# Kernel optimization log

Hardware: AMD Instinct MI355X
Metric: run time of the kernel (lower is better)

Reference implementation:

```python
import jax, jax.numpy as jnp
import numpy as np

SL, BS, OUT_SL = 64, 64, 48
NH, EME, EMD = 256, 512, 768   # em_sz_dec == 3*NH required by copy-score reshape/bmm
VE, VD = 32000, 32000
NL = 2


def setup_inputs() -> dict:
    key = jax.random.key(0)
    ks = iter(jax.random.split(key, 32))
    def W(*s, sc=0.05):
        return jax.random.normal(next(ks), s, jnp.float32) * sc
    inp = jax.random.randint(next(ks), (SL, BS), 0, VE)
    y = jax.random.randint(next(ks), (SL, BS), 0, VD)
    return dict(
        inp=inp, y=y,
        emb_enc=W(VE, EME, sc=0.1),
        enc_Wih=W(NL, 2, 3 * NH, EME), enc_Whh=W(NL, 2, 3 * NH, NH),
        enc_bih=W(NL, 2, 3 * NH), enc_bhh=W(NL, 2, 3 * NH),
        out_enc_W=W(EMD, 2 * NH),
        emb_dec=W(VD, EMD, sc=0.1),
        dec_Wih=W(NL, 3 * EMD, EMD), dec_Whh=W(NL, 3 * EMD, EMD),
        dec_bih=W(NL, 3 * EMD), dec_bhh=W(NL, 3 * EMD),
        out_b=W(VD),
        W1=W(2 * NH, EMD), l2_W=W(EMD, EMD), l2_b=W(EMD),
        l3_W=W(EMD, EMD + 2 * NH), l3_b=W(EMD),
        Vp=W(EMD),
    )


def _gru_cell(x, h, Wih, Whh, bih, bhh):
    # torch nn.GRU cell equations
    gi = x @ Wih.T + bih
    gh = h @ Whh.T + bhh
    ir, iz, inn = jnp.split(gi, 3, axis=-1)
    hr, hz, hn = jnp.split(gh, 3, axis=-1)
    r = jax.nn.sigmoid(ir + hr)
    z = jax.nn.sigmoid(iz + hz)
    n = jnp.tanh(inn + r * hn)
    return (1.0 - z) * n + z * h


def _gru_layer(xs, h0, Wih, Whh, bih, bhh, reverse=False):
    def step(h, x):
        h2 = _gru_cell(x, h, Wih, Whh, bih, bhh)
        return h2, h2
    hT, ys = jax.lax.scan(step, h0, xs, reverse=reverse)
    return ys, hT


def reference(inp, y, emb_enc, enc_Wih, enc_Whh, enc_bih, enc_bhh, out_enc_W,
              emb_dec, dec_Wih, dec_Whh, dec_bih, dec_bhh, out_b,
              W1, l2_W, l2_b, l3_W, l3_b, Vp):
    sl, bs = inp.shape
    # ---- encoder: 2-layer bidirectional GRU ----
    x = emb_enc[inp]                                   # (sl, bs, EME)
    h_fin = []
    for l in range(NL):
        yf, hf = _gru_layer(x, jnp.zeros((bs, NH), x.dtype),
                            enc_Wih[l, 0], enc_Whh[l, 0], enc_bih[l, 0], enc_bhh[l, 0])
        yb, hb = _gru_layer(x, jnp.zeros((bs, NH), x.dtype),
                            enc_Wih[l, 1], enc_Whh[l, 1], enc_bih[l, 1], enc_bhh[l, 1],
                            reverse=True)
        x = jnp.concatenate([yf, yb], -1)              # (sl, bs, 2*NH)
        h_fin.append(jnp.concatenate([hf, hb], -1))    # (bs, 2*NH)
    enc_out = x
    # h.view(2,2,bs,-1).permute(0,2,1,3).view(2,bs,-1) == per-layer [fwd,bwd] concat
    h = jnp.stack(h_fin) @ out_enc_W.T                 # (2, bs, EMD)

    w1e = enc_out @ W1                                 # (sl, bs, EMD)
    sc_base = jnp.tanh(enc_out @ out_enc_W.T).transpose(1, 0, 2)  # (bs, sl, EMD)
    yT = y.T                                           # (bs, sl) copy indices
    Vsz = emb_dec.shape[0]
    row = jnp.arange(bs)[:, None]
    # dec_inp: step 0 uses zeros token, then teacher-forced y[i-1]
    dec_inputs = jnp.concatenate([jnp.zeros((1, bs), y.dtype), y[:OUT_SL - 1]], 0)

    def step(h, dec_t):
        # Bahdanau attention
        w2h = h[-1] @ l2_W.T + l2_b                    # (bs, EMD)
        u = jnp.tanh(w1e + w2h[None])                  # (sl, bs, EMD)
        a = jax.nn.softmax(u @ Vp, axis=0)             # (sl, bs)
        Xa = jnp.einsum('sb,sbe->be', a, enc_out)      # (bs, 2*NH)
        e = emb_dec[dec_t]                             # (bs, EMD)
        wgt = jnp.concatenate([e, Xa], -1) @ l3_W.T + l3_b
        # 2-layer decoder GRU, single step
        h0n = _gru_cell(wgt, h[0], dec_Wih[0], dec_Whh[0], dec_bih[0], dec_bhh[0])
        h1n = _gru_cell(h0n, h[1], dec_Wih[1], dec_Whh[1], dec_bih[1], dec_bhh[1])
        hn = jnp.stack([h0n, h1n])
        dec_out = h1n                                  # (bs, EMD)
        outp = dec_out @ emb_dec.T + out_b             # generate scores (bs, VD), tied weights
        score_c = jnp.tanh(jnp.einsum('bse,be->bs', sc_base, dec_out))  # copy scores (bs, sl)
        probs = jax.nn.softmax(jnp.concatenate([outp, score_c], 1), axis=1)  # (bs, VD+sl)
        prob_g = probs[:, :Vsz]
        prob_c = probs[:, Vsz:]
        # scatter-add copy probs onto the token ids of y (the copy mechanism)
        out1 = jnp.zeros_like(probs).at[row, yT].add(prob_c)
        out1 = out1.at[:, :Vsz].add(prob_g)
        return hn, out1

    _, res = jax.lax.scan(step, h, dec_inputs)         # (OUT_SL, bs, VD+sl)
    return res
```

## Files before the change

kernel.cpp:

```cpp
#include <hip/hip_runtime.h>

#define SLEN 64
#define BSZ  64
#define TSL  48
#define VDIM 32000
#define NCOL 32064

typedef __attribute__((ext_vector_type(8))) _Float16 f16x8;
typedef __attribute__((ext_vector_type(4))) _Float16 f16x4;
typedef __attribute__((ext_vector_type(4))) float f32x4;

__device__ __forceinline__ float fsig(float x){
    return 1.0f/(1.0f + __expf(-x));
}
__device__ __forceinline__ float ftanh(float x){
    float e = __expf(2.0f*x);
    return 1.0f - 2.0f/(e + 1.0f);
}
__device__ __forceinline__ unsigned short f2h(float x){
    union { _Float16 f; unsigned short u; } c; c.f = (_Float16)x; return c.u;
}
__device__ __forceinline__ float h2f(unsigned short u){
    union { _Float16 f; unsigned short u; } c; c.u = u; return (float)c.f;
}
__device__ __forceinline__ unsigned short f2h_hi(float x, float& rem){
    _Float16 h = (_Float16)x;
    rem = x - (float)h;
    union { _Float16 f; unsigned short u; } c; c.f = h; return c.u;
}
__device__ __forceinline__ float gru_fuse(float gir,float giz,float gin,
                                          float ghr,float ghz,float ghn,float h){
    float r = fsig(gir + ghr);
    float z = fsig(giz + ghz);
    float n = ftanh(gin + r*ghn);
    return (1.0f - z)*n + z*h;
}

__global__ __launch_bounds__(256) void mfma_gemm(
    const float* A0, const unsigned short* Bh0, const unsigned short* Bl0,
    const float* bias0, float* C0, int N0, int ldc0, int act0,
    const float* A1, const unsigned short* Bh1, const unsigned short* Bl1,
    const float* bias1, float* C1, int N1, int ldc1, int act1,
    int K, int c16)
{
    const float* A; const unsigned short* Bh; const unsigned short* Bl;
    const float* bias; float* C; int N, ldc, act;
    if (blockIdx.z == 0) { A=A0; Bh=Bh0; Bl=Bl0; bias=bias0; C=C0; N=N0; ldc=ldc0; act=act0; }
    else                 { A=A1; Bh=Bh1; Bl=Bl1; bias=bias1; C=C1; N=N1; ldc=ldc1; act=act1; }

    const int n0 = blockIdx.x * 128;
    if (n0 >= N) return;
    const int m0 = blockIdx.y * 64;

    __shared__ __align__(16) unsigned short As[2][64][72];
    __shared__ __align__(16) unsigned short Bs[2][128][72];

    const int t  = threadIdx.x;
    const int wv = t >> 6, ln = t & 63;
    const bool has_lo = (Bl != nullptr);

    f32x4 acc[4][2];
    #pragma unroll
    for (int i = 0; i < 4; ++i)
        #pragma unroll
        for (int j = 0; j < 2; ++j) acc[i][j] = (f32x4){0.f,0.f,0.f,0.f};

    for (int k0 = 0; k0 < K; k0 += 64) {
        __syncthreads();
        #pragma unroll
        for (int it = 0; it < 4; ++it) {
            int idx = t + it*256;
            int r = idx >> 4, c4 = (idx & 15) * 4;
            float4 v = *reinterpret_cast<const float4*>(A + (size_t)(m0+r)*K + k0 + c4);
            ushort4 h, l; float rm;
            h.x = f2h_hi(v.x, rm); l.x = f2h(rm);
            h.y = f2h_hi(v.y, rm); l.y = f2h(rm);
            h.z = f2h_hi(v.z, rm); l.z = f2h(rm);
            h.w = f2h_hi(v.w, rm); l.w = f2h(rm);
            *reinterpret_cast<ushort4*>(&As[0][r][c4]) = h;
            *reinterpret_cast<ushort4*>(&As[1][r][c4]) = l;
        }
        #pragma unroll
        for (int it = 0; it < 4; ++it) {
            int idx = t + it*256;
            int r = idx >> 3, c8 = (idx & 7) * 8;
            *reinterpret_cast<uint4*>(&Bs[0][r][c8]) =
                *reinterpret_cast<const uint4*>(&Bh[(size_t)(n0+r)*K + k0 + c8]);
        }
        if (has_lo) {
            #pragma unroll
            for (int it = 0; it < 4; ++it) {
                int idx = t + it*256;
                int r = idx >> 3, c8 = (idx & 7) * 8;
                *reinterpret_cast<uint4*>(&Bs[1][r][c8]) =
                    *reinterpret_cast<const uint4*>(&Bl[(size_t)(n0+r)*K + k0 + c8]);
            }
        }
        __syncthreads();
        #pragma unroll
        for (int ks = 0; ks < 2; ++ks) {
            const int ko = ks*32 + (ln >> 4)*8;
            f16x8 ah[4], al[4], bh[2], bl[2];
            #pragma unroll
            for (int m = 0; m < 4; ++m) {
                ah[m] = *reinterpret_cast<const f16x8*>(&As[0][m*16 + (ln&15)][ko]);
                al[m] = *reinterpret_cast<const f16x8*>(&As[1][m*16 + (ln&15)][ko]);
            }
            #pragma unroll
            for (int n = 0; n < 2; ++n) {
                bh[n] = *reinterpret_cast<const f16x8*>(&Bs[0][wv*32 + n*16 + (ln&15)][ko]);
                if (has_lo)
                    bl[n] = *reinterpret_cast<const f16x8*>(&Bs[1][wv*32 + n*16 + (ln&15)][ko]);
            }
            #pragma unroll
            for (int m = 0; m < 4; ++m)
                #pragma unroll
                for (int n = 0; n < 2; ++n) {
                    acc[m][n] = __builtin_amdgcn_mfma_f32_16x16x32_f16(ah[m], bh[n], acc[m][n], 0,0,0);
                    acc[m][n] = __builtin_amdgcn_mfma_f32_16x16x32_f16(al[m], bh[n], acc[m][n], 0,0,0);
                    if (has_lo)
                        acc[m][n] = __builtin_amdgcn_mfma_f32_16x16x32_f16(ah[m], bl[n], acc[m][n], 0,0,0);
                }
        }
    }
    #pragma unroll
    for (int m = 0; m < 4; ++m) {
        #pragma unroll
        for (int n = 0; n < 2; ++n) {
            const int col = n0 + wv*32 + n*16 + (ln & 15);
            const float bz = bias ? bias[col] : 0.0f;
            #pragma unroll
            for (int j = 0; j < 4; ++j) {
                const int row = m0 + m*16 + (ln >> 4)*4 + j;
                float v = acc[m][n][j] + bz;
                if (act) v = ftanh(v);
                if (c16) ((unsigned short*)C)[(size_t)row*ldc + col] = f2h(v);
                else     C[(size_t)row*ldc + col] = v;
            }
        }
    }
}

__global__ __launch_bounds__(256) void packwhh_k(
    const float* __restrict__ Whh, unsigned short* __restrict__ P)
{
    int gidx = blockIdx.x*256 + threadIdx.x;
    if (gidx >= 2*3*32*256) return;
    int col = gidx & 255;
    int k8  = (gidx >> 8) & 31;
    int g   = (gidx >> 13) % 3;
    int d   = gidx / (3*32*256);
    const float* src = Whh + ((size_t)(d*768 + g*256 + col))*256 + k8*8;
    ushort4 lo4, hi4;
    float4 v0 = *reinterpret_cast<const float4*>(src);
    float4 v1 = *reinterpret_cast<const float4*>(src + 4);
    lo4.x = f2h(v0.x); lo4.y = f2h(v0.y); lo4.z = f2h(v0.z); lo4.w = f2h(v0.w);
    hi4.x = f2h(v1.x); hi4.y = f2h(v1.y); hi4.z = f2h(v1.z); hi4.w = f2h(v1.w);
    reinterpret_cast<ushort4*>(P + (size_t)gidx*8)[0] = lo4;
    reinterpret_cast<ushort4*>(P + (size_t)gidx*8)[1] = hi4;
}

__global__ __launch_bounds__(512) void enc_cp5_k(
    const float* __restrict__ giF, const float* __restrict__ giB,
    const unsigned short* __restrict__ Wp,
    const float* __restrict__ bhh,
    float* __restrict__ yout, float* __restrict__ hfin, int permute)
{
    const int b = blockIdx.x, d = blockIdx.y, t = threadIdx.x;
    const int c  = t & 255;
    const int kh = t >> 8;
    const float* gi_base = d ? giB : giF;
    const unsigned short* W = Wp + (size_t)d*3*32*256*8;
    const float br  = bhh[d*768 + c];
    const float bz2 = bhh[d*768 + c + 256];
    const float bn  = bhh[d*768 + c + 512];

    __shared__ float hsA[256];
    __shared__ float hsB[256];
    __shared__ float red[3][256];
    if (kh == 0) hsA[c] = 0.0f;

    float gr = 0.f, gz = 0.f, gn = 0.f, h_own = 0.f;
    if (kh == 0) {
        const int s0 = d ? 63 : 0;
        const float* gip0 = gi_base + (size_t)(s0*64 + b)*768;
        gr = gip0[c]; gz = gip0[c+256]; gn = gip0[c+512];
    }
    __syncthreads();

    for (int step = 0; step < 64; ++step) {
        const int s = d ? (63 - step) : step;
        float ngr = 0.f, ngz = 0.f, ngn = 0.f;
        if (kh == 0 && step < 63) {
            const int sn = d ? (62 - step) : (step + 1);
            const float* gip = gi_base + (size_t)(sn*64 + b)*768;
            ngr = gip[c]; ngz = gip[c+256]; ngn = gip[c+512];
        }
        const float* hs = (step & 1) ? hsB : hsA;
        float*       hw = (step & 1) ? hsA : hsB;

        float ar = 0.f, az = 0.f, an = 0.f;
        const int kb = kh * 16;
        #pragma unroll 8
        for (int k8i = 0; k8i < 16; ++k8i) {
            const int k8 = kb + k8i;
            f16x8 wr = *reinterpret_cast<const f16x8*>(W + ((size_t)(0*32 + k8)*256 + c)*8);
            f16x8 wz = *reinterpret_cast<const f16x8*>(W + ((size_t)(1*32 + k8)*256 + c)*8);
            f16x8 wn = *reinterpret_cast<const f16x8*>(W + ((size_t)(2*32 + k8)*256 + c)*8);
            float4 h0 = *reinterpret_cast<const float4*>(&hs[k8*8]);
            float4 h1 = *reinterpret_cast<const float4*>(&hs[k8*8+4]);
            ar += h0.x*(float)wr[0] + h0.y*(float)wr[1] + h0.z*(float)wr[2] + h0.w*(float)wr[3]
                + h1.x*(float)wr[4] + h1.y*(float)wr[5] + h1.z*(float)wr[6] + h1.w*(float)wr[7];
            az += h0.x*(float)wz[0] + h0.y*(float)wz[1] + h0.z*(float)wz[2] + h0.w*(float)wz[3]
                + h1.x*(float)wz[4] + h1.y*(float)wz[5] + h1.z*(float)wz[6] + h1.w*(float)wz[7];
            an += h0.x*(float)wn[0] + h0.y*(float)wn[1] + h0.z*(float)wn[2] + h0.w*(float)wn[3]
                + h1.x*(float)wn[4] + h1.y*(float)wn[5] + h1.z*(float)wn[6] + h1.w*(float)wn[7];
        }
        if (kh == 1) { red[0][c] = ar; red[1][c] = az; red[2][c] = an; }
        __syncthreads();
        if (kh == 0) {
            ar += red[0][c]; az += red[1][c]; an += red[2][c];
            float r  = fsig(gr + ar + br);
            float z  = fsig(gz + az + bz2);
            float n  = ftanh(gn + r*(an + bn));
            float hn2 = (1.0f - z)*n + z*h_own;
            h_own = hn2;
            hw[c] = hn2;
            const int idx = permute ? (b*64 + s) : (s*64 + b);
            yout[(size_t)idx*512 + d*256 + c] = hn2;
            gr = ngr; gz = ngz; gn = ngn;
        }
        __syncthreads();
    }
    if (kh == 0) hfin[(size_t)b*512 + d*256 + c] = h_own;
}

__global__ __launch_bounds__(512) void gru_mfma_k(
    const float* A0, const unsigned short* BH0, const unsigned short* BL0,
    const float* bias0, const float* gh0, const float* hold0, float* out0,
    int gate0, int K0, const unsigned short* E0,
    const float* A1, const unsigned short* BH1, const unsigned short* BL1,
    const float* bias1, const float* gh1, const float* hold1, float* out1,
    int gate1, int K1, const unsigned short* E1, float* psz)
{
    const float* A; const unsigned short* BH; const unsigned short* BL;
    const float* bias; const float* gh; const float* hold; float* outp; int gate, K;
    const unsigned short* E;
    if (blockIdx.z == 0) { A=A0; BH=BH0; BL=BL0; bias=bias0; gh=gh0; hold=hold0; outp=out0; gate=gate0; K=K0; E=E0; }
    else                 { A=A1; BH=BH1; BL=BL1; bias=bias1; gh=gh1; hold=hold1; outp=out1; gate=gate1; K=K1; E=E1; }

    const int t = threadIdx.x;
    if (psz && blockIdx.z == 0 && blockIdx.x == 0) psz[t] = 0.f;
    const int w  = t >> 6, ln = t & 63;
    const int rw = w & 3;
    const int kh = w >> 2;
    const int colg16 = blockIdx.x * 16;
    const int arow = rw*16 + (ln & 15);
    const int kof  = (ln >> 4) * 8;
    const bool has_lo = (BL != nullptr);

    f32x4 acc[3];
    #pragma unroll
    for (int g = 0; g < 3; ++g) acc[g] = (f32x4){0.f,0.f,0.f,0.f};

    const float* Ar = A + (size_t)arow*K + kof;
    const int brow_n = colg16 + (ln & 15);
    const int Khalf = K >> 1;
    const int kbeg = kh * Khalf;

    #pragma unroll 2
    for (int k0 = kbeg; k0 < kbeg + Khalf; k0 += 32) {
        float4 a0 = *reinterpret_cast<const float4*>(Ar + k0);
        float4 a1 = *reinterpret_cast<const float4*>(Ar + k0 + 4);
        f16x8 ah, al;
        {
            float av0=a0.x, av1=a0.y, av2=a0.z, av3=a0.w;
            float av4=a1.x, av5=a1.y, av6=a1.z, av7=a1.w;
            _Float16 hh;
            hh=(_Float16)av0; ah[0]=hh; al[0]=(_Float16)(av0-(float)hh);
            hh=(_Float16)av1; ah[1]=hh; al[1]=(_Float16)(av1-(float)hh);
            hh=(_Float16)av2; ah[2]=hh; al[2]=(_Float16)(av2-(float)hh);
            hh=(_Float16)av3; ah[3]=hh; al[3]=(_Float16)(av3-(float)hh);
            hh=(_Float16)av4; ah[4]=hh; al[4]=(_Float16)(av4-(float)hh);
            hh=(_Float16)av5; ah[5]=hh; al[5]=(_Float16)(av5-(float)hh);
            hh=(_Float16)av6; ah[6]=hh; al[6]=(_Float16)(av6-(float)hh);
            hh=(_Float16)av7; ah[7]=hh; al[7]=(_Float16)(av7-(float)hh);
        }
        #pragma unroll
        for (int g = 0; g < 3; ++g) {
            const size_t boff = (size_t)(g*768 + brow_n)*K + k0 + kof;
            f16x8 bh = *reinterpret_cast<const f16x8*>(&BH[boff]);
            acc[g] = __builtin_amdgcn_mfma_f32_16x16x32_f16(ah, bh, acc[g], 0,0,0);
            acc[g] = __builtin_amdgcn_mfma_f32_16x16x32_f16(al, bh, acc[g], 0,0,0);
            if (has_lo) {
                f16x8 bl = *reinterpret_cast<const f16x8*>(&BL[boff]);
                acc[g] = __builtin_amdgcn_mfma_f32_16x16x32_f16(ah, bl, acc[g], 0,0,0);
            }
        }
    }

    __shared__ float red[4][64][12];
    if (kh == 1) {
        #pragma unroll
        for (int g = 0; g < 3; ++g)
            #pragma unroll
            for (int j = 0; j < 4; ++j) red[rw][ln][g*4 + j] = acc[g][j];
    }
    __syncthreads();
    if (kh == 1) return;
    #pragma unroll
    for (int g = 0; g < 3; ++g)
        #pragma unroll
        for (int j = 0; j < 4; ++j) acc[g][j] += red[rw][ln][g*4 + j];

    const int colg = colg16 + (ln & 15);
    const int rb   = rw*16 + (ln >> 4)*4;
    if (gate) {
        const float br = bias[colg], bz = bias[768+colg], bn = bias[1536+colg];
        #pragma unroll
        for (int jj = 0; jj < 4; ++jj) {
            const int row = rb + jj;
            float er = 0.f, ez = 0.f, en = 0.f;
            if (E) {
                er = h2f(E[(size_t)row*2304 + colg]);
                ez = h2f(E[(size_t)row*2304 + 768 + colg]);
                en = h2f(E[(size_t)row*2304 + 1536 + colg]);
            }
            float ghr = gh[(size_t)row*2304 + colg];
            float ghz = gh[(size_t)row*2304 + 768 + colg];
            float ghn = gh[(size_t)row*2304 + 1536 + colg];
            float h   = hold[(size_t)row*768 + colg];
            outp[(size_t)row*768 + colg] =
                gru_fuse(acc[0][jj]+br+er, acc[1][jj]+bz+ez, acc[2][jj]+bn+en, ghr, ghz, ghn, h);
        }
    } else {
        #pragma unroll
        for (int g = 0; g < 3; ++g) {
            const float bz = bias[g*768 + colg];
            #pragma unroll
            for (int jj = 0; jj < 4; ++jj)
                outp[(size_t)(rb+jj)*2304 + g*768 + colg] = acc[g][jj] + bz;
        }
    }
}

__global__ __launch_bounds__(512) void vocab4_k(
    const float* __restrict__ A,
    const unsigned short* __restrict__ B0, const float* __restrict__ bias0,
    unsigned short* __restrict__ scr16, float* __restrict__ psum,
    const unsigned short* __restrict__ B1, const float* __restrict__ bias1, float* __restrict__ C1,
    const unsigned short* __restrict__ B2, const float* __restrict__ bias2, float* __restrict__ C2,
    const unsigned short* __restrict__ scb16, float* __restrict__ cpt)
{
    const int z = blockIdx.z;
    const int t = threadIdx.x, w = t >> 6, ln = t & 63;

    if (z == 3) {
        const int b = blockIdx.x;
        if (b >= 64) return;
        __shared__ float hsh[768];
        for (int i = t; i < 768; i += 512) hsh[i] = A[(size_t)b*768 + i];
        __syncthreads();
        for (int ss = 0; ss < 8; ++ss) {
            const int s = w*8 + ss;
            const unsigned short* sp = scb16 + (size_t)(b*64 + s)*768;
            float acc = 0.f;
            #pragma unroll
            for (int q = 0; q < 6; ++q) {
                int e = ln*2 + q*128;
                unsigned u = *reinterpret_cast<const unsigned*>(&sp[e]);
                acc += h2f((unsigned short)(u & 0xffff))*hsh[e]
                     + h2f((unsigned short)(u >> 16))*hsh[e+1];
            }
            for (int off = 32; off; off >>= 1) acc += __shfl_down(acc, off);
            if (ln == 0) cpt[b*64 + s] = ftanh(acc);
        }
        return;
    }

    const unsigned short* Bh; const float* bias; int N, ldc;
    if (z == 0)      { Bh=B0; bias=bias0; N=VDIM; ldc=VDIM; }
    else if (z == 1) { Bh=B1; bias=bias1; N=768;  ldc=768; }
    else             { Bh=B2; bias=bias2; N=2304; ldc=2304; }
    const int n0 = blockIdx.x * 128;
    if (n0 >= N) return;

    __shared__ __align__(16) unsigned short As[2][64][72];
    __shared__ __align__(16) unsigned short Bs[128][72];
    __shared__ float rs[4][64];

    const int cw = w & 3;
    const int mh = w >> 2;

    f32x4 acc[2][2];
    #pragma unroll
    for (int i = 0; i < 2; ++i)
        #pragma unroll
        for (int j = 0; j < 2; ++j) acc[i][j] = (f32x4){0.f,0.f,0.f,0.f};

    for (int k0 = 0; k0 < 768; k0 += 64) {
        __syncthreads();
        #pragma unroll
        for (int it = 0; it < 2; ++it) {
            int idx = t + it*512;
            int r = idx >> 4, c4 = (idx & 15) * 4;
            float4 v = *reinterpret_cast<const float4*>(A + (size_t)r*768 + k0 + c4);
            ushort4 h, l; float rm;
            h.x = f2h_hi(v.x, rm); l.x = f2h(rm);
            h.y = f2h_hi(v.y, rm); l.y = f2h(rm);
            h.z = f2h_hi(v.z, rm); l.z = f2h(rm);
            h.w = f2h_hi(v.w, rm); l.w = f2h(rm);
            *reinterpret_cast<ushort4*>(&As[0][r][c4]) = h;
            *reinterpret_cast<ushort4*>(&As[1][r][c4]) = l;
        }
        #pragma unroll
        for (int it = 0; it < 2; ++it) {
            int idx = t + it*512;
            int r = idx >> 3, c8 = (idx & 7) * 8;
            *reinterpret_cast<uint4*>(&Bs[r][c8]) =
                *reinterpret_cast<const uint4*>(&Bh[(size_t)(n0+r)*768 + k0 + c8]);
        }
        __syncthreads();
        #pragma unroll
        for (int ks = 0; ks < 2; ++ks) {
            const int ko = ks*32 + (ln >> 4)*8;
            f16x8 ah[2], al[2], bh[2];
            #pragma unroll
            for (int m = 0; m < 2; ++m) {
                ah[m] = *reinterpret_cast<const f16x8*>(&As[0][mh*32 + m*16 + (ln&15)][ko]);
                al[m] = *reinterpret_cast<const f16x8*>(&As[1][mh*32 + m*16 + (ln&15)][ko]);
            }
            #pragma unroll
            for (int n = 0; n < 2; ++n)
                bh[n] = *reinterpret_cast<const f16x8*>(&Bs[cw*32 + n*16 + (ln&15)][ko]);
            #pragma unroll
            for (int m = 0; m < 2; ++m)
                #pragma unroll
                for (int n = 0; n < 2; ++n) {
                    acc[m][n] = __builtin_amdgcn_mfma_f32_16x16x32_f16(ah[m], bh[n], acc[m][n], 0,0,0);
                    acc[m][n] = __builtin_amdgcn_mfma_f32_16x16x32_f16(al[m], bh[n], acc[m][n], 0,0,0);
                }
        }
    }

    if (z == 0) {
        __syncthreads();
        unsigned short (*Cs)[128] = reinterpret_cast<unsigned short(*)[128]>(&As[0][0][0]);
        float sums[2][4];
        #pragma unroll
        for (int m = 0; m < 2; ++m)
            #pragma unroll
            for (int j = 0; j < 4; ++j) sums[m][j] = 0.f;
        #pragma unroll
        for (int m = 0; m < 2; ++m) {
            #pragma unroll
            for (int n = 0; n < 2; ++n) {
                const int cl = cw*32 + n*16 + (ln & 15);
                const float bz = bias[n0 + cl];
                #pragma unroll
                for (int j = 0; j < 4; ++j) {
                    const int row = mh*32 + m*16 + (ln >> 4)*4 + j;
                    float e = __expf(acc[m][n][j] + bz);
                    Cs[row][cl] = f2h(e);
                    sums[m][j] += e;
                }
            }
        }
        #pragma unroll
        for (int m = 0; m < 2; ++m)
            #pragma unroll
            for (int j = 0; j < 4; ++j) {
                float v = sums[m][j];
                v += __shfl_xor(v, 1); v += __shfl_xor(v, 2);
                v += __shfl_xor(v, 4); v += __shfl_xor(v, 8);
                if ((ln & 15) == 0)
                    rs[cw][mh*32 + m*16 + (ln >> 4)*4 + j] = v;
            }
        __syncthreads();
        #pragma unroll
        for (int it = 0; it < 2; ++it) {
            int jj = t + it*512;
            int row = jj >> 4, c8 = (jj & 15) * 8;
            *reinterpret_cast<uint4*>(&scr16[(size_t)row*VDIM + n0 + c8]) =
                *reinterpret_cast<const uint4*>(&Cs[row][c8]);
        }
        if (t < 64)
            atomicAdd(&psum[t*8 + (blockIdx.x & 7)], rs[0][t]+rs[1][t]+rs[2][t]+rs[3][t]);
    } else {
        float* C = (z == 1) ? C1 : C2;
        #pragma unroll
        for (int m = 0; m < 2; ++m) {
            #pragma unroll
            for (int n = 0; n < 2; ++n) {
                const int col = n0 + cw*32 + n*16 + (ln & 15);
                const float bz = bias[col];
                #pragma unroll
                for (int j = 0; j < 4; ++j) {
                    const int row = mh*32 + m*16 + (ln >> 4)*4 + j;
                    C[(size_t)row*ldc + col] = acc[m][n][j] + bz;
                }
            }
        }
    }
}

__global__ __launch_bounds__(512) void attsm_k(
    const unsigned short* __restrict__ w1e16, const float* __restrict__ w2h,
    const float* __restrict__ Vp, const unsigned short* __restrict__ enc16,
    const int* __restrict__ y,
    int step, int do_att, int do_sm,
    float* __restrict__ wgt_in,
    const unsigned short* __restrict__ scr16, const float* __restrict__ cpt,
    const float* __restrict__ psum, float* __restrict__ outprev)
{
    const int b = blockIdx.x, t = threadIdx.x;
    const int w = t >> 6, ln = t & 63;
    if (blockIdx.y == 0) {
        if (!do_att) return;
        __shared__ float w2s[768];
        __shared__ float vps[768];
        __shared__ float aa[64];
        for (int i = t; i < 768; i += 512) { w2s[i] = w2h[(size_t)b*768 + i]; vps[i] = Vp[i]; }
        __syncthreads();
        for (int ss = 0; ss < 8; ++ss) {
            const int s = w*8 + ss;
            const unsigned short* wrow = w1e16 + (size_t)(b*64 + s)*768;
            float acc = 0.f;
            #pragma unroll
            for (int q = 0; q < 6; ++q) {
                int e = ln*2 + q*128;
                unsigned u = *reinterpret_cast<const unsigned*>(&wrow[e]);
                acc += ftanh(h2f((unsigned short)(u & 0xffff)) + w2s[e])*vps[e]
                     + ftanh(h2f((unsigned short)(u >> 16))   + w2s[e+1])*vps[e+1];
            }
            for (int off = 32; off; off >>= 1) acc += __shfl_down(acc, off);
            if (ln == 0) aa[s] = acc;
        }
        __syncthreads();
        if (t < 64) {
            float v = aa[t];
            float m = v;
            for (int off = 32; off; off >>= 1) m = fmaxf(m, __shfl_xor(m, off));
            float e = __expf(v - m);
            float ssum = e;
            for (int off = 32; off; off >>= 1) ssum += __shfl_xor(ssum, off);
            aa[t] = e / ssum;
        }
        __syncthreads();
        {
            float a0 = 0.f;
            const unsigned short* ebase = enc16 + (size_t)(b*64)*512 + t;
            #pragma unroll 8
            for (int s = 0; s < 64; ++s)
                a0 += aa[s] * h2f(ebase[(size_t)s*512]);
            wgt_in[(size_t)b*512 + t] = a0;
        }
    } else {
        if (!do_sm) return;
        __shared__ float cps[64];
        __shared__ float invS;
        if (t < 64) cps[t] = __expf(cpt[b*64 + t]);
        __syncthreads();
        if (t < 64) {
            float v = cps[t];
            for (int off = 32; off; off >>= 1) v += __shfl_xor(v, off);
            if (t == 0) {
                float tot = v;
                #pragma unroll
                for (int k = 0; k < 8; ++k) tot += psum[b*8 + k];
                invS = 1.0f / tot;
            }
        }
        __syncthreads();
        const float inv = invS;
        const unsigned short* srow = scr16 + (size_t)b*VDIM;
        float* orow = outprev + (size_t)b*NCOL;
        for (int i = t*8; i < VDIM; i += 4096) {
            uint4 u = *reinterpret_cast<const uint4*>(&srow[i]);
            float4 o0, o1;
            o0.x = h2f((unsigned short)(u.x & 0xffff))*inv; o0.y = h2f((unsigned short)(u.x >> 16))*inv;
            o0.z = h2f((unsigned short)(u.y & 0xffff))*inv; o0.w = h2f((unsigned short)(u.y >> 16))*inv;
            o1.x = h2f((unsigned short)(u.z & 0xffff))*inv; o1.y = h2f((unsigned short)(u.z >> 16))*inv;
            o1.z = h2f((unsigned short)(u.w & 0xffff))*inv; o1.w = h2f((unsigned short)(u.w >> 16))*inv;
            *reinterpret_cast<float4*>(&orow[i])     = o0;
            *reinterpret_cast<float4*>(&orow[i + 4]) = o1;
        }
        if (t >= 448) orow[VDIM + (t - 448)] = 0.0f;
        __syncthreads();
        if (t < 64) atomicAdd(&orow[y[t*64 + b]], cps[t] * inv);
    }
}

__global__ __launch_bounds__(256) void convhl_k(
    const float* __restrict__ W, unsigned short* __restrict__ hi,
    unsigned short* __restrict__ lo, int n4)
{
    int i = blockIdx.x*256 + threadIdx.x;
    if (i >= n4) return;
    float4 v = reinterpret_cast<const float4*>(W)[i];
    ushort4 h, l; float r;
    h.x = f2h_hi(v.x, r); l.x = f2h(r);
    h.y = f2h_hi(v.y, r); l.y = f2h(r);
    h.z = f2h_hi(v.z, r); l.z = f2h(r);
    h.w = f2h_hi(v.w, r); l.w = f2h(r);
    reinterpret_cast<ushort4*>(hi)[i] = h;
    reinterpret_cast<ushort4*>(lo)[i] = l;
}
__global__ __launch_bounds__(256) void conv16_k(
    const float* __restrict__ W, unsigned short* __restrict__ hi, int n4)
{
    int i = blockIdx.x*256 + threadIdx.x;
    if (i >= n4) return;
    float4 v = reinterpret_cast<const float4*>(W)[i];
    ushort4 h;
    h.x = f2h(v.x); h.y = f2h(v.y); h.z = f2h(v.z); h.w = f2h(v.w);
    reinterpret_cast<ushort4*>(hi)[i] = h;
}
__global__ __launch_bounds__(256) void convw03_k(
    const float* __restrict__ W03f, unsigned short* __restrict__ We,
    unsigned short* __restrict__ Wx)
{
    int i = blockIdx.x*256 + threadIdx.x;
    if (i >= 2304*320) return;
    int r = i / 320, c4 = (i - r*320) * 4;
    float4 v = *reinterpret_cast<const float4*>(W03f + (size_t)r*1280 + c4);
    ushort4 h;
    h.x = f2h(v.x); h.y = f2h(v.y); h.z = f2h(v.z); h.w = f2h(v.w);
    if (c4 < 768)
        *reinterpret_cast<ushort4*>(&We[(size_t)r*768 + c4]) = h;
    else
        *reinterpret_cast<ushort4*>(&Wx[(size_t)r*512 + (c4 - 768)]) = h;
}
__global__ __launch_bounds__(256) void embrows_k(
    const int* __restrict__ y, const float* __restrict__ emb_dec,
    float* __restrict__ Ag)
{
    int i = blockIdx.x*256 + threadIdx.x;
    if (i >= 3072*192) return;
    int row = i / 192, c4 = (i - row*192) * 4;
    int tok = (row < 64) ? 0 : y[row - 64];
    *reinterpret_cast<float4*>(Ag + (size_t)row*768 + c4) =
        *reinterpret_cast<const float4*>(emb_dec + (size_t)tok*768 + c4);
// ... 265 lines not shown
__global__ __launch_bounds__(256) void smax2_k(
    const float* __restrict__ scratch, const float* __restrict__ scb,
    const float* __restrict__ h1, const int* __restrict__ y, float* __restrict__ out)
{
    const int b = blockIdx.x, t = threadIdx.x;
    __shared__ float hsh[768];
    __shared__ float cps[64];
    __shared__ float red[4];
    for (int i = t; i < 768; i += 256) hsh[i] = h1[(size_t)b*768 + i];
    __syncthreads();
    const int wv = t >> 6, ln = t & 63;
    for (int ss = 0; ss < 16; ++ss) {
        const int s = wv*16 + ss;
        const float* sp = scb + (size_t)(b*64 + s)*768;
        float acc = 0.f;
        #pragma unroll
        for (int q = 0; q < 12; ++q) { int e = ln + q*64; acc += sp[e]*hsh[e]; }
        for (int off = 32; off; off >>= 1) acc += __shfl_down(acc, off);
        if (ln == 0) cps[s] = ftanh(acc);
    }
    __syncthreads();

    const float* row = scratch + (size_t)b*VDIM;
    float m = -1e30f;
    for (int i = t; i < VDIM; i += 256) m = fmaxf(m, row[i]);
    for (int off = 32; off; off >>= 1) m = fmaxf(m, __shfl_xor(m, off));
    if (ln == 0) red[wv] = m;
    __syncthreads();
    const float bm = fmaxf(fmaxf(red[0], red[1]), fmaxf(red[2], red[3]));
    __syncthreads();

    float s = 0.f;
    for (int i = t; i < VDIM; i += 256) s += __expf(row[i] - bm);
    if (t < 64) s += __expf(cps[t] - bm);
    for (int off = 32; off; off >>= 1) s += __shfl_xor(s, off);
    if (ln == 0) red[wv] = s;
    __syncthreads();
    const float inv = 1.0f / (red[0] + red[1] + red[2] + red[3]);

    float* orow = out + (size_t)b*NCOL;
    for (int i = t; i < VDIM; i += 256) orow[i] = __expf(row[i] - bm) * inv;
    if (t >= 192) orow[VDIM + (t - 192)] = 0.0f;
    __syncthreads();
    if (t < 64) atomicAdd(&orow[y[t*64 + b]], __expf(cps[t] - bm) * inv);
}

extern "C" void kernel_launch(void* const* d_in, const int* in_sizes, int n_in,
                              void* d_out, int out_size, void* d_ws, size_t ws_size,
                              hipStream_t stream)
{
    (void)in_sizes; (void)n_in; (void)out_size;
    const int*   inp       = (const int*)  d_in[0];
    const int*   y         = (const int*)  d_in[1];
    const float* emb_enc   = (const float*)d_in[2];
    const float* enc_Wih   = (const float*)d_in[3];
    const float* enc_Whh   = (const float*)d_in[4];
    const float* enc_bih   = (const float*)d_in[5];
    const float* enc_bhh   = (const float*)d_in[6];
    const float* out_enc_W = (const float*)d_in[7];
    const float* emb_dec   = (const float*)d_in[8];
    const float* dec_Wih   = (const float*)d_in[9];
    const float* dec_Whh   = (const float*)d_in[10];
    const float* dec_bih   = (const float*)d_in[11];
    const float* dec_bhh   = (const float*)d_in[12];
    const float* out_b     = (const float*)d_in[13];
    const float* W1        = (const float*)d_in[14];
    const float* l2_W      = (const float*)d_in[15];
    const float* l2_b      = (const float*)d_in[16];
    const float* l3_W      = (const float*)d_in[17];
    const float* l3_b      = (const float*)d_in[18];
    const float* Vp        = (const float*)d_in[19];
    float* out = (float*)d_out;
    float* ws  = (float*)d_ws;

    size_t off = 0;
    auto alloc = [&](size_t n) { float* p = ws + off; off += (n + 63) & ~(size_t)63; return p; };
    float* x0     = alloc(4096*512);
    float* x1     = alloc(4096*512);
    float* x2     = alloc(4096*512);
    float* giF    = alloc(4096*768);
    float* giB    = alloc(4096*768);
    float* w1e    = alloc(4096*768);
    float* scb    = alloc(4096*768);
    float* W1T    = alloc(768*512);
    float* hfin   = alloc(128*512);
    float* hdecA  = alloc(128*768);
    float* hdecB  = alloc(128*768);
    float* w2h    = alloc(64*768);
    float* wgt_in = alloc(64*1280);
    float* wgt    = alloc(64*768);
    float* gh0buf = alloc(64*2304);
    float* gh1buf = alloc(64*2304);
    float* gi0f   = alloc(64*2304);
    float* gi1f   = alloc(64*2304);
    float* b03    = alloc(2304);
    float* psum   = alloc(1024);
    float* cpt    = alloc(2*4096);
    float* scratch= alloc(64*VDIM);
    auto ualloc = [&](size_t nush) { return (unsigned short*)alloc((nush + 1) / 2); };
    unsigned short* encWhhH = ualloc(2*2*768*256);
    unsigned short* encWhhP = ualloc(2*3*32*256*8);
    unsigned short* embH    = ualloc((size_t)VDIM*768);
    unsigned short* encWihH = ualloc(2*2*768*512);
    unsigned short* encWihL = ualloc(2*2*768*512);
    unsigned short* W1TH    = ualloc(768*512);
    unsigned short* W1TL    = ualloc(768*512);
    unsigned short* oeH     = ualloc(768*512);
    unsigned short* oeL     = ualloc(768*512);
    unsigned short* l2H     = ualloc(768*768);
    unsigned short* l3TH    = ualloc(1280*768);
    unsigned short* l3TL    = ualloc(1280*768);
    unsigned short* dWihH   = ualloc((size_t)2*2304*768);
    unsigned short* dWhhH   = ualloc((size_t)2*2304*768);
    unsigned short* W03eH   = ualloc((size_t)2304*768);
    unsigned short* W03xH   = ualloc((size_t)2304*512);
    unsigned short* Egi16   = ualloc((size_t)3072*2304);
    const bool use_mfma = ws_size >= off * sizeof(float);

    const size_t L1W = (size_t)2304*768;
    const size_t SCR = (size_t)64*VDIM;
    float* l3T  = scratch;
    float* W03f = x0;
    float* Ag   = x0;
    unsigned short* scr16 = (unsigned short*)scratch;
    unsigned short* w1e16 = (unsigned short*)giF;
    unsigned short* enc16 = (unsigned short*)(giF + 1600*1024);
    unsigned short* scb16 = (unsigned short*)giB;

    embed_k<<<2048, 256, 0, stream>>>(inp, emb_enc, x0);
    transpose2_k<<<(512*768 + 255)/256, 256, 0, stream>>>(W1, W1T, 512, 768);
    conv16_k<<<768, 256, 0, stream>>>(enc_Whh, encWhhH, 2*2*768*256/4);

    if (use_mfma) {
        packwhh_k<<<192, 256, 0, stream>>>(enc_Whh, encWhhP);
        convhl_k<<<1536, 256, 0, stream>>>(enc_Wih, encWihH, encWihL, 2*2*768*512/4);
        convhl_k<<<384, 256, 0, stream>>>(W1T, W1TH, W1TL, 768*512/4);
        convhl_k<<<384, 256, 0, stream>>>(out_enc_W, oeH, oeL, 768*512/4);
        conv16_k<<<576, 256, 0, stream>>>(l2_W, l2H, 768*768/4);
        conv16_k<<<3456, 256, 0, stream>>>(dec_Wih, dWihH, (int)(L1W*2/4));
        conv16_k<<<3456, 256, 0, stream>>>(dec_Whh, dWhhH, (int)(L1W*2/4));
        conv16_k<<<24000, 256, 0, stream>>>(emb_dec, embH, (int)((size_t)VDIM*768/4));
        transpose2_k<<<(768*1280 + 255)/256, 256, 0, stream>>>(l3_W, l3T, 768, 1280);
        convhl_k<<<960, 256, 0, stream>>>(l3T, l3TH, l3TL, 1280*768/4);
        b03_k<<<9, 256, 0, stream>>>(dec_Wih, dec_bih, l3_b, b03);

        for (int l = 0; l < 2; ++l) {
            const float* xin  = l ? x1 : x0;
            float*       xout = l ? x2 : x1;
            const size_t wo = (size_t)l*2*768*512;
            mfma_gemm<<<dim3(6, 64, 2), 256, 0, stream>>>(
                xin, encWihH + wo,           encWihL + wo,           enc_bih + l*2*768,       giF, 768, 768, 0,
                xin, encWihH + wo + 768*512, encWihL + wo + 768*512, enc_bih + l*2*768 + 768, giB, 768, 768, 0,
                512, 0);
            enc_cp5_k<<<dim3(64, 2), 512, 0, stream>>>(
                giF, giB, encWhhP, enc_bhh + (size_t)l*2*768,
                xout, hfin + (size_t)l*64*512, l);
            if (l == 0)
                packwhh_k<<<192, 256, 0, stream>>>(enc_Whh + (size_t)2*768*256, encWhhP);
        }

        mfma_gemm<<<dim3(10, 36, 1), 256, 0, stream>>>(
            dec_Wih, l3TH, l3TL, nullptr, W03f, 1280, 1280, 0,
            nullptr, nullptr, nullptr, nullptr, nullptr, 0, 0, 0,
            768, 0);
        convw03_k<<<(2304*320 + 255)/256, 256, 0, stream>>>(W03f, W03eH, W03xH);

        embrows_k<<<(3072*192 + 255)/256, 256, 0, stream>>>(y, emb_dec, Ag);
        mfma_gemm<<<dim3(18, 48, 1), 256, 0, stream>>>(
            Ag, W03eH, nullptr, nullptr, (float*)Egi16, 2304, 2304, 0,
            nullptr, nullptr, nullptr, nullptr, nullptr, 0, 0, 0,
            768, 1);

        mfma_gemm<<<dim3(6, 2, 1), 256, 0, stream>>>(
            hfin, oeH, oeL, nullptr, hdecA, 768, 768, 0,
            nullptr, nullptr, nullptr, nullptr, nullptr, 0, 0, 0,
            512, 0);

        mfma_gemm<<<dim3(6, 64, 2), 256, 0, stream>>>(
            x2, W1TH, W1TL, nullptr, w1e, 768, 768, 0,
            x2, oeH,  oeL,  nullptr, scb, 768, 768, 1,
            512, 0);

        conv16_k<<<3072, 256, 0, stream>>>(w1e, w1e16, 4096*768/4);
        conv16_k<<<3072, 256, 0, stream>>>(scb, scb16, 4096*768/4);
        conv16_k<<<2048, 256, 0, stream>>>(x2, enc16, 4096*512/4);

        mfma_gemm<<<dim3(6, 1, 1), 256, 0, stream>>>(
            hdecA + 64*768, l2H, nullptr, l2_b, w2h, 768, 768, 0,
            nullptr, nullptr, nullptr, nullptr, nullptr, 0, 0, 0,
            768, 0);
        gru_mfma_k<<<dim3(48, 1, 2), 512, 0, stream>>>(
            hdecA,          dWhhH,       nullptr, dec_bhh,        nullptr, nullptr, gh0buf, 0, 768, nullptr,
            hdecA + 64*768, dWhhH + L1W, nullptr, dec_bhh + 2304, nullptr, nullptr, gh1buf, 0, 768, nullptr,
            nullptr);

        for (int st = 0; st < TSL; ++st) {
            float* h0c = (st & 1) ? hdecB : hdecA;
            float* h0n = (st & 1) ? hdecA : hdecB;
            float* h1c = h0c + 64*768;
            float* h1n = h0n + 64*768;
            float* oprev = out + (size_t)(st > 0 ? st - 1 : 0)*BSZ*NCOL;

            attsm_k<<<dim3(64, 2), 512, 0, stream>>>(
                w1e16, w2h, Vp, enc16, y, st, 1, (st > 0) ? 1 : 0,
                wgt_in, scr16, cpt, psum, oprev);

            gru_mfma_k<<<dim3(48, 1, 1), 512, 0, stream>>>(
                wgt_in, W03xH, nullptr, b03, gh0buf, h0c, h0n, 1, 512, Egi16 + (size_t)st*64*2304,
                wgt_in, W03xH, nullptr, b03, gh0buf, h0c, h0n, 1, 512, Egi16 + (size_t)st*64*2304,
                psum);

            gru_mfma_k<<<dim3(48, 1, 2), 512, 0, stream>>>(
                h0n, dWihH + L1W, nullptr, dec_bih + 2304, gh1buf, h1c, h1n, 1, 768, nullptr,
                h0n, dWhhH,       nullptr, dec_bhh,        nullptr, nullptr, gh0buf, 0, 768, nullptr,
                nullptr);

            vocab4_k<<<dim3(250, 1, 4), 512, 0, stream>>>(
                h1n,
                embH, out_b, scr16, psum,
                l2H, l2_b, w2h,
                dWhhH + L1W, dec_bhh + 2304, gh1buf,
                scb16, cpt);
        }
        attsm_k<<<dim3(64, 2), 512, 0, stream>>>(
            w1e16, w2h, Vp, enc16, y, TSL, 0, 1,
            wgt_in, scr16, cpt, psum, out + (size_t)(TSL-1)*BSZ*NCOL);
    } else {
        for (int l = 0; l < 2; ++l) {
            const float* xin  = l ? x1 : x0;
            float*       xout = l ? x2 : x1;
            const float* Wih = enc_Wih + (size_t)l*2*768*512;
            const float* bih = enc_bih + (size_t)l*2*768;
            gemm64<<<dim3(12, 64, 2), 256, 0, stream>>>(
                xin, Wih,           bih,       giF, 0,
                xin, Wih + 768*512, bih + 768, giB, 0,
                4096, 768, 512, 768);
            enc_layer4_k<<<dim3(16, 2), 256, 0, stream>>>(
                giF, giB, encWhhH + (size_t)l*2*768*256, enc_bhh + (size_t)l*2*768,
                xout, hfin + (size_t)l*64*512, l);
        }
        gemm64<<<dim3(12, 2, 1), 256, 0, stream>>>(
            hfin, out_enc_W, nullptr, hdecA, 0,
            hfin, out_enc_W, nullptr, hdecA, 0,
            128, 768, 512, 768);
        gemm64<<<dim3(12, 64, 2), 256, 0, stream>>>(
            x2, W1T,       nullptr, w1e, 0,
            x2, out_enc_W, nullptr, scb, 1,
            4096, 768, 512, 768);
        gemm_skinny<<<dim3(12, 4, 1), 256, 0, stream>>>(
            hdecA + 64*768, l2_W, l2_b, w2h,
            hdecA + 64*768, l2_W, l2_b, w2h,
            768, 768, 768);

        for (int st = 0; st < TSL; ++st) {
            float* h0c = (st & 1) ? hdecB : hdecA;
            float* h0n = (st & 1) ? hdecA : hdecB;
            float* h1c = h0c + 64*768;
            float* h1n = h0n + 64*768;
            float* orow = out + (size_t)st*BSZ*NCOL;

            att_fused_k<<<64, 256, 0, stream>>>(w1e, w2h, Vp, x2, emb_dec, y, st, wgt_in);
            gemm_skinny<<<dim3(12, 4, 1), 256, 0, stream>>>(
                wgt_in, l3_W, l3_b, wgt,
                wgt_in, l3_W, l3_b, wgt,
                768, 1280, 768);
            gemm_skinny<<<dim3(36, 4, 2), 256, 0, stream>>>(
                wgt, dec_Wih, dec_bih, gi0f,
                h0c, dec_Whh, dec_bhh, gh0buf,
                2304, 768, 2304);
            gru_gate_k<<<192, 256, 0, stream>>>(gi0f, gh0buf, h0c, h0n);
            gemm_skinny<<<dim3(36, 4, 2), 256, 0, stream>>>(
                h0n, dec_Wih + L1W, dec_bih + 2304, gi1f,
                h1c, dec_Whh + L1W, dec_bhh + 2304, gh1buf,
                2304, 768, 2304);
            gru_gate_k<<<192, 256, 0, stream>>>(gi1f, gh1buf, h1c, h1n);
            gemm_skinny<<<dim3(12, 4, 1), 256, 0, stream>>>(
                h1n, l2_W, l2_b, w2h,
                h1n, l2_W, l2_b, w2h,
                768, 768, 768);
            gemm64<<<dim3(500, 1, 1), 256, 0, stream>>>(
                h1n, emb_dec, out_b, scratch, 0,
                h1n, emb_dec, out_b, scratch, 0,
                64, VDIM, 768, VDIM);
            smax2_k<<<64, 256, 0, stream>>>(scratch, scb, h1n, y, orow);
        }
    }
}
```

Baseline: 4.706 ms.

## Split encoder GRU recurrence over four K-quarters and move layer-0 hidden GEMM into vocab kernel

The encoder recurrence kernel now runs 1024 threads per block, splitting the K dimension four ways with a three-slot shared reduction instead of two ways, which shortens the serial per-step dot-product chain. In the decoder loop, the layer-0 hidden-to-hidden projection (h0n·Whh for the next step) is removed from the second gru_mfma launch and handled by a fifth z-slice of the vocab kernel, so it overlaps with the vocab GEMM. This halves the grid of the layer-1 GRU launch. The cost is more shared-memory reduction work and higher register pressure at 1024 threads in the encoder.

```diff
diff --git a/kernel.cpp b/kernel.cpp
--- a/kernel.cpp
+++ b/kernel.cpp
@@ -160,7 +160,7 @@
     reinterpret_cast<ushort4*>(P + (size_t)gidx*8)[1] = hi4;
 }
 
-__global__ __launch_bounds__(512) void enc_cp5_k(
+__global__ __launch_bounds__(1024) void enc_cp6_k(
     const float* __restrict__ giF, const float* __restrict__ giB,
     const unsigned short* __restrict__ Wp,
     const float* __restrict__ bhh,
@@ -168,7 +168,7 @@
 {
     const int b = blockIdx.x, d = blockIdx.y, t = threadIdx.x;
     const int c  = t & 255;
-    const int kh = t >> 8;
+    const int kq = t >> 8;
     const float* gi_base = d ? giB : giF;
     const unsigned short* W = Wp + (size_t)d*3*32*256*8;
     const float br  = bhh[d*768 + c];
@@ -177,11 +177,11 @@
 
     __shared__ float hsA[256];
     __shared__ float hsB[256];
-    __shared__ float red[3][256];
-    if (kh == 0) hsA[c] = 0.0f;
+    __shared__ float red[3][3][256];
+    if (t < 256) hsA[t] = 0.0f;
 
     float gr = 0.f, gz = 0.f, gn = 0.f, h_own = 0.f;
-    if (kh == 0) {
+    if (kq == 0) {
         const int s0 = d ? 63 : 0;
         const float* gip0 = gi_base + (size_t)(s0*64 + b)*768;
         gr = gip0[c]; gz = gip0[c+256]; gn = gip0[c+512];
@@ -191,7 +191,7 @@
     for (int step = 0; step < 64; ++step) {
         const int s = d ? (63 - step) : step;
         float ngr = 0.f, ngz = 0.f, ngn = 0.f;
-        if (kh == 0 && step < 63) {
+        if (kq == 0 && step < 63) {
             const int sn = d ? (62 - step) : (step + 1);
             const float* gip = gi_base + (size_t)(sn*64 + b)*768;
             ngr = gip[c]; ngz = gip[c+256]; ngn = gip[c+512];
@@ -200,9 +200,9 @@
         float*       hw = (step & 1) ? hsA : hsB;
 
         float ar = 0.f, az = 0.f, an = 0.f;
-        const int kb = kh * 16;
+        const int kb = kq * 8;
         #pragma unroll 8
-        for (int k8i = 0; k8i < 16; ++k8i) {
+        for (int k8i = 0; k8i < 8; ++k8i) {
             const int k8 = kb + k8i;
             f16x8 wr = *reinterpret_cast<const f16x8*>(W + ((size_t)(0*32 + k8)*256 + c)*8);
             f16x8 wz = *reinterpret_cast<const f16x8*>(W + ((size_t)(1*32 + k8)*256 + c)*8);
@@ -216,10 +216,16 @@
             an += h0.x*(float)wn[0] + h0.y*(float)wn[1] + h0.z*(float)wn[2] + h0.w*(float)wn[3]
                 + h1.x*(float)wn[4] + h1.y*(float)wn[5] + h1.z*(float)wn[6] + h1.w*(float)wn[7];
         }
-        if (kh == 1) { red[0][c] = ar; red[1][c] = az; red[2][c] = an; }
-        __syncthreads();
-        if (kh == 0) {
-            ar += red[0][c]; az += red[1][c]; an += red[2][c];
+        if (kq != 0) {
+            red[kq-1][0][c] = ar;
+            red[kq-1][1][c] = az;
+            red[kq-1][2][c] = an;
+        }
+        __syncthreads();
+        if (kq == 0) {
+            ar += red[0][0][c] + red[1][0][c] + red[2][0][c];
+            az += red[0][1][c] + red[1][1][c] + red[2][1][c];
+            an += red[0][2][c] + red[1][2][c] + red[2][2][c];
             float r  = fsig(gr + ar + br);
             float z  = fsig(gz + az + bz2);
             float n  = ftanh(gn + r*(an + bn));
@@ -232,7 +238,7 @@
         }
         __syncthreads();
     }
-    if (kh == 0) hfin[(size_t)b*512 + d*256 + c] = h_own;
+    if (kq == 0) hfin[(size_t)b*512 + d*256 + c] = h_own;
 }
 
 __global__ __launch_bounds__(512) void gru_mfma_k(
@@ -344,13 +350,15 @@
     }
 }
 
-__global__ __launch_bounds__(512) void vocab4_k(
+__global__ __launch_bounds__(512) void vocab5_k(
     const float* __restrict__ A,
     const unsigned short* __restrict__ B0, const float* __restrict__ bias0,
     unsigned short* __restrict__ scr16, float* __restrict__ psum,
     const unsigned short* __restrict__ B1, const float* __restrict__ bias1, float* __restrict__ C1,
     const unsigned short* __restrict__ B2, const float* __restrict__ bias2, float* __restrict__ C2,
-    const unsigned short* __restrict__ scb16, float* __restrict__ cpt)
+    const unsigned short* __restrict__ scb16, float* __restrict__ cpt,
+    const float* __restrict__ A4,
+    const unsigned short* __restrict__ B4, const float* __restrict__ bias4, float* __restrict__ C4)
 {
     const int z = blockIdx.z;
     const int t = threadIdx.x, w = t >> 6, ln = t & 63;
@@ -378,10 +386,12 @@
         return;
     }
 
+    const float* Ap = (z == 4) ? A4 : A;
     const unsigned short* Bh; const float* bias; int N, ldc;
     if (z == 0)      { Bh=B0; bias=bias0; N=VDIM; ldc=VDIM; }
     else if (z == 1) { Bh=B1; bias=bias1; N=768;  ldc=768; }
-    else             { Bh=B2; bias=bias2; N=2304; ldc=2304; }
+    else if (z == 2) { Bh=B2; bias=bias2; N=2304; ldc=2304; }
+    else             { Bh=B4; bias=bias4; N=2304; ldc=2304; }
     const int n0 = blockIdx.x * 128;
     if (n0 >= N) return;
 
@@ -404,7 +414,7 @@
         for (int it = 0; it < 2; ++it) {
             int idx = t + it*512;
             int r = idx >> 4, c4 = (idx & 15) * 4;
-            float4 v = *reinterpret_cast<const float4*>(A + (size_t)r*768 + k0 + c4);
+            float4 v = *reinterpret_cast<const float4*>(Ap + (size_t)r*768 + k0 + c4);
             ushort4 h, l; float rm;
             h.x = f2h_hi(v.x, rm); l.x = f2h(rm);
             h.y = f2h_hi(v.y, rm); l.y = f2h(rm);
@@ -487,7 +497,7 @@
         if (t < 64)
             atomicAdd(&psum[t*8 + (blockIdx.x & 7)], rs[0][t]+rs[1][t]+rs[2][t]+rs[3][t]);
     } else {
-        float* C = (z == 1) ? C1 : C2;
+        float* C = (z == 1) ? C1 : ((z == 2) ? C2 : C4);
         #pragma unroll
         for (int m = 0; m < 2; ++m) {
             #pragma unroll
@@ -1059,7 +1069,7 @@
                 xin, encWihH + wo,           encWihL + wo,           enc_bih + l*2*768,       giF, 768, 768, 0,
                 xin, encWihH + wo + 768*512, encWihL + wo + 768*512, enc_bih + l*2*768 + 768, giB, 768, 768, 0,
                 512, 0);
-            enc_cp5_k<<<dim3(64, 2), 512, 0, stream>>>(
+            enc_cp6_k<<<dim3(64, 2), 1024, 0, stream>>>(
                 giF, giB, encWhhP, enc_bhh + (size_t)l*2*768,
                 xout, hfin + (size_t)l*64*512, l);
             if (l == 0)
@@ -1117,17 +1127,18 @@
                 wgt_in, W03xH, nullptr, b03, gh0buf, h0c, h0n, 1, 512, Egi16 + (size_t)st*64*2304,
                 psum);
 
-            gru_mfma_k<<<dim3(48, 1, 2), 512, 0, stream>>>(
+            gru_mfma_k<<<dim3(48, 1, 1), 512, 0, stream>>>(
                 h0n, dWihH + L1W, nullptr, dec_bih + 2304, gh1buf, h1c, h1n, 1, 768, nullptr,
-                h0n, dWhhH,       nullptr, dec_bhh,        nullptr, nullptr, gh0buf, 0, 768, nullptr,
+                h0n, dWihH + L1W, nullptr, dec_bih + 2304, gh1buf, h1c, h1n, 1, 768, nullptr,
                 nullptr);
 
-            vocab4_k<<<dim3(250, 1, 4), 512, 0, stream>>>(
+            vocab5_k<<<dim3(250, 1, 5), 512, 0, stream>>>(
                 h1n,
                 embH, out_b, scr16, psum,
                 l2H, l2_b, w2h,
                 dWhhH + L1W, dec_bhh + 2304, gh1buf,
-                scb16, cpt);
+                scb16, cpt,
+                h0n, dWhhH, dec_bhh, gh0buf);
         }
         attsm_k<<<dim3(64, 2), 512, 0, stream>>>(
             w1e16, w2h, Vp, enc16, y, TSL, 0, 1,
```

Result: slower. 8.038 ms (+70.8%).
